# Kernel optimization log

Hardware: AMD Instinct MI355X
Metric: run time of the kernel (lower is better)

The kernel has to match this reference:

```python
import jax, jax.numpy as jnp
import numpy as np

N = 100000   # nodes
E = 1600000  # edges
IN = 32
HID = 64
OUT = 1

def setup_inputs() -> dict:
    key = jax.random.key(0)
    ks = jax.random.split(key, 16)
    x = jax.random.normal(ks[0], (N, IN), jnp.float32)
    edge_index = jax.random.randint(ks[1], (2, E), 0, N, dtype=jnp.int32)
    def lin(k, fi, fo):
        return jax.random.normal(k, (fi, fo), jnp.float32) / np.sqrt(fi)
    # SAGEConv params per layer: Wn/bn for aggregated neighbors (lin_l), Wr for root (lin_r, no bias)
    Wn0 = lin(ks[2], IN, HID);  bn0 = jnp.zeros((HID,), jnp.float32); Wr0 = lin(ks[3], IN, HID)
    Wn1 = lin(ks[4], HID, HID); bn1 = jnp.zeros((HID,), jnp.float32); Wr1 = lin(ks[5], HID, HID)
    Wn2 = lin(ks[6], HID, HID); bn2 = jnp.zeros((HID,), jnp.float32); Wr2 = lin(ks[7], HID, HID)
    # predictor MLP
    Wp1 = lin(ks[8], HID, HID); bp1 = jnp.zeros((HID,), jnp.float32)
    Wp2 = lin(ks[9], HID, OUT); bp2 = jnp.zeros((OUT,), jnp.float32)
    return dict(x=x, edge_index=edge_index,
                Wn0=Wn0, bn0=bn0, Wr0=Wr0,
                Wn1=Wn1, bn1=bn1, Wr1=Wr1,
                Wn2=Wn2, bn2=bn2, Wr2=Wr2,
                Wp1=Wp1, bp1=bp1, Wp2=Wp2, bp2=bp2)

def reference(x, edge_index, Wn0, bn0, Wr0, Wn1, bn1, Wr1, Wn2, bn2, Wr2, Wp1, bp1, Wp2, bp2):
    src, dst = edge_index[0], edge_index[1]
    n = x.shape[0]
    # mean-aggregation normalization (nodes with no in-edges get 0, as in PyG)
    cnt = jax.ops.segment_sum(jnp.ones(src.shape, x.dtype), dst, num_segments=n)
    inv = jnp.where(cnt > 0, 1.0 / jnp.maximum(cnt, 1.0), 0.0)[:, None]

    def sage(h, Wn, bn, Wr):
        agg = jax.ops.segment_sum(h[src], dst, num_segments=n) * inv  # [N, d]
        return agg @ Wn + bn + h @ Wr

    h = jax.nn.relu(sage(x, Wn0, bn0, Wr0))
    h = jax.nn.relu(sage(h, Wn1, bn1, Wr1))
    h = sage(h, Wn2, bn2, Wr2)  # no activation after last GNN layer
    h = jax.nn.relu(h @ Wp1 + bp1)
    return jax.nn.sigmoid(h @ Wp2 + bp2)
```

## Files before the change

### kernel.cpp

```cpp
#include <hip/hip_runtime.h>
#include <math.h>

#define NN 100000
#define EE 1600000
#define HID 64
#define BKT 391
#define SLAB 5504
#define CHUNK 4096
#define NWG ((EE + CHUNK - 1) / CHUNK)

typedef _Float16 f16;
typedef _Float16 f16x2 __attribute__((ext_vector_type(2)));

__device__ __forceinline__ f16x2 u2h(unsigned u) { return __builtin_bit_cast(f16x2, u); }
__device__ __forceinline__ unsigned h2u(f16x2 h) { return __builtin_bit_cast(unsigned, h); }

#if defined(__has_builtin) && __has_builtin(__builtin_amdgcn_fdot2)
__device__ __forceinline__ float dot2(f16x2 a, f16x2 b, float c) {
    return __builtin_amdgcn_fdot2(a, b, c, false);
}
#else
__device__ __forceinline__ float dot2(f16x2 a, f16x2 b, float c) {
    c = fmaf((float)a.x, (float)b.x, c);
    return fmaf((float)a.y, (float)b.y, c);
}
#endif


__global__ void place_kernel(const int* __restrict__ src, const int* __restrict__ dst,
                             int* __restrict__ bfill, unsigned* __restrict__ pairs) {
    __shared__ int lc[BKT];
    __shared__ int lbase[BKT];
    int t = threadIdx.x;
    for (int b = t; b < BKT; b += 256) lc[b] = 0;
    __syncthreads();
    int base = blockIdx.x * CHUNK;
    int myd[CHUNK / 256];
#pragma unroll
    for (int j = 0; j < CHUNK / 256; ++j) {
        int i = base + j * 256 + t;
        myd[j] = (i < EE) ? dst[i] : -1;
        if (myd[j] >= 0) atomicAdd(&lc[myd[j] >> 8], 1);
    }
    __syncthreads();
    for (int b = t; b < BKT; b += 256) {
        int c = lc[b];
        if (c) {
            int ofs = atomicAdd(&bfill[b], c);
            if (ofs + c > SLAB) ofs = SLAB - c;
            lbase[b] = b * SLAB + ofs;
        }
    }
    __syncthreads();
    for (int b = t; b < BKT; b += 256) lc[b] = 0;
    __syncthreads();
#pragma unroll
    for (int j = 0; j < CHUNK / 256; ++j) {
        int i = base + j * 256 + t;
        if (myd[j] >= 0) {
            int b = myd[j] >> 8;
            int r = atomicAdd(&lc[b], 1);
            pairs[lbase[b] + r] = (unsigned)src[i] | ((unsigned)(myd[j] & 255) << 24);
        }
    }
}

__global__ void build_kernel(const unsigned* __restrict__ pairs,
                             const int* __restrict__ bfill,
                             int* __restrict__ rs, int* __restrict__ re,
                             float* __restrict__ inv, int* __restrict__ col) {
    __shared__ unsigned s_pk[SLAB];
    __shared__ int ncnt[256];
    __shared__ int nexcl[256];
    int b = blockIdx.x;
    int t = threadIdx.x;
    int s0 = b * SLAB;
    int ce = bfill[b]; if (ce > SLAB) ce = SLAB;
    ncnt[t] = 0;
    for (int e = t; e < ce; e += 256) s_pk[e] = pairs[s0 + e];
    __syncthreads();
    for (int e = t; e < ce; e += 256) atomicAdd(&ncnt[s_pk[e] >> 24], 1);
    __syncthreads();
    int c = ncnt[t];
    nexcl[t] = c;
    __syncthreads();
    for (int off = 1; off < 256; off <<= 1) {
        int u = (t >= off) ? nexcl[t - off] : 0;
        __syncthreads();
        nexcl[t] += u;
        __syncthreads();
    }
    int excl = nexcl[t] - c;
    int node = (b << 8) + t;
    if (node < NN) {
        rs[node] = s0 + excl;
        re[node] = s0 + excl + c;
        inv[node] = (c > 0) ? (1.0f / (float)c) : 0.0f;
    }
    __syncthreads();
    nexcl[t] = excl;
    ncnt[t] = 0;
    __syncthreads();
    for (int e = t; e < ce; e += 256) {
        unsigned pk = s_pk[e];
        int d = pk >> 24;
        int r = atomicAdd(&ncnt[d], 1);
        col[s0 + nexcl[d] + r] = (int)(pk & 0xFFFFFFu);
    }
}


__global__ void transform32_kernel(const float* __restrict__ h,
                                   const float* __restrict__ Wn,
                                   const float* __restrict__ bn,
                                   const float* __restrict__ Wr,
                                   f16* __restrict__ hn,
                                   f16* __restrict__ hrb,
                                   const float* __restrict__ Wn1,
                                   const float* __restrict__ Wr1,
                                   const float* __restrict__ Wn2,
                                   const float* __restrict__ Wr2,
                                   const float* __restrict__ Wp1,
                                   unsigned* __restrict__ w16) {
    if (blockIdx.x < 40) {
        int id = blockIdx.x * 256 + threadIdx.x;
        int mat = id >> 11;
        int p = (id >> 6) & 31;
        int j = id & 63;
        const float* W = (mat == 0) ? Wn1 : (mat == 1) ? Wr1 :
                         (mat == 2) ? Wn2 : (mat == 3) ? Wr2 : Wp1;
        f16x2 v;
        v.x = (f16)W[(2 * p) * HID + j];
        v.y = (f16)W[(2 * p + 1) * HID + j];
        w16[id] = h2u(v);
    }

    int lane = threadIdx.x & 63;
    int wid = (blockIdx.x * blockDim.x + threadIdx.x) >> 6;
    int m0 = __builtin_amdgcn_readfirstlane(wid << 2);
    const float* h0 = h + (size_t)m0 * 32;

    float an0 = 0.f, an1 = 0.f, an2 = 0.f, an3 = 0.f;
    float ar0 = 0.f, ar1 = 0.f, ar2 = 0.f, ar3 = 0.f;
#pragma unroll
    for (int k = 0; k < 32; ++k) {
        float wn = Wn[k * HID + lane];
        float wr = Wr[k * HID + lane];
        float hk0 = h0[k], hk1 = h0[32 + k], hk2 = h0[64 + k], hk3 = h0[96 + k];
        an0 = fmaf(hk0, wn, an0); ar0 = fmaf(hk0, wr, ar0);
        an1 = fmaf(hk1, wn, an1); ar1 = fmaf(hk1, wr, ar1);
        an2 = fmaf(hk2, wn, an2); ar2 = fmaf(hk2, wr, ar2);
        an3 = fmaf(hk3, wn, an3); ar3 = fmaf(hk3, wr, ar3);
    }
    float b = bn[lane];
    size_t o = (size_t)m0 * HID + lane;
    hn[o] = (f16)an0; hn[o + HID] = (f16)an1;
    hn[o + 2 * HID] = (f16)an2; hn[o + 3 * HID] = (f16)an3;
    hrb[o] = (f16)(ar0 + b); hrb[o + HID] = (f16)(ar1 + b);
    hrb[o + 2 * HID] = (f16)(ar2 + b); hrb[o + 3 * HID] = (f16)(ar3 + b);
}


__device__ __forceinline__ void qgather(const uint2* __restrict__ rp,
                                        const int* __restrict__ col,
                                        int e, int en, int fl,
                                        f16x2& s0, f16x2& s1) {
    while (e + 16 <= en) {
        int c[16];
#pragma unroll
        for (int i = 0; i < 16; ++i) c[i] = col[e + i];
        uint2 v[16];
#pragma unroll
        for (int i = 0; i < 16; ++i) v[i] = rp[(size_t)c[i] * 16 + fl];
#pragma unroll
        for (int i = 0; i < 16; ++i) { s0 += u2h(v[i].x); s1 += u2h(v[i].y); }
        e += 16;
    }
    if (e + 8 <= en) {
        int c[8];
#pragma unroll
        for (int i = 0; i < 8; ++i) c[i] = col[e + i];
        uint2 v[8];
#pragma unroll
        for (int i = 0; i < 8; ++i) v[i] = rp[(size_t)c[i] * 16 + fl];
#pragma unroll
        for (int i = 0; i < 8; ++i) { s0 += u2h(v[i].x); s1 += u2h(v[i].y); }
        e += 8;
    }
    if (e + 4 <= en) {
        int c0 = col[e], c1 = col[e + 1], c2 = col[e + 2], c3 = col[e + 3];
        uint2 v0 = rp[(size_t)c0 * 16 + fl];
        uint2 v1 = rp[(size_t)c1 * 16 + fl];
        uint2 v2 = rp[(size_t)c2 * 16 + fl];
        uint2 v3 = rp[(size_t)c3 * 16 + fl];
        s0 += u2h(v0.x); s1 += u2h(v0.y);
        s0 += u2h(v1.x); s1 += u2h(v1.y);
        s0 += u2h(v2.x); s1 += u2h(v2.y);
        s0 += u2h(v3.x); s1 += u2h(v3.y);
        e += 4;
    }
    while (e < en) {
        uint2 v = rp[(size_t)col[e] * 16 + fl];
        s0 += u2h(v.x); s1 += u2h(v.y);
        ++e;
    }
}


__global__ void gt_kernel(const f16* __restrict__ An,
                          const int* __restrict__ rs, const int* __restrict__ re,
                          const int* __restrict__ col, const float* __restrict__ inv,
                          f16* C,
                          const unsigned* __restrict__ Wn16, const float* __restrict__ bn,
                          const unsigned* __restrict__ Wr16,
                          f16* __restrict__ Aout) {
    int lane = threadIdx.x & 63;
    int wid = (blockIdx.x * blockDim.x + threadIdx.x) >> 6;
    int m0 = wid << 2;
    int m = m0 + (lane >> 4);
    int fl = lane & 15;

    f16x2 s0 = (f16x2)0, s1 = (f16x2)0;
    qgather((const uint2*)An, col, rs[m], re[m], fl, s0, s1);

    float iv = inv[m];
    uint2 cur = ((const uint2*)C)[(size_t)m * 16 + fl];
    f16x2 q0 = u2h(cur.x), q1 = u2h(cur.y);
    f16x2 hA, hB;
    hA.x = (f16)fmaxf(fmaf((float)s0.x, iv, (float)q0.x), 0.f);
    hA.y = (f16)fmaxf(fmaf((float)s0.y, iv, (float)q0.y), 0.f);
    hB.x = (f16)fmaxf(fmaf((float)s1.x, iv, (float)q1.x), 0.f);
    hB.y = (f16)fmaxf(fmaf((float)s1.y, iv, (float)q1.y), 0.f);
    unsigned hx = h2u(hA), hy = h2u(hB);

    float an[4] = {0.f, 0.f, 0.f, 0.f};
    float ar[4] = {0.f, 0.f, 0.f, 0.f};
#pragma unroll
    for (int kk = 0; kk < 16; ++kk) {
        f16x2 wnA = u2h(Wn16[(2 * kk) * HID + lane]);
        f16x2 wnB = u2h(Wn16[(2 * kk + 1) * HID + lane]);
        f16x2 wrA = u2h(Wr16[(2 * kk) * HID + lane]);
        f16x2 wrB = u2h(Wr16[(2 * kk + 1) * HID + lane]);
#pragma unroll
        for (int n = 0; n < 4; ++n) {
            f16x2 px = u2h(__shfl(hx, (n << 4) + kk));
            f16x2 py = u2h(__shfl(hy, (n << 4) + kk));
            an[n] = dot2(px, wnA, an[n]);
            an[n] = dot2(py, wnB, an[n]);
            ar[n] = dot2(px, wrA, ar[n]);
            ar[n] = dot2(py, wrB, ar[n]);
        }
    }
    float b = bn[lane];
    size_t o = (size_t)m0 * HID + lane;
#pragma unroll
    for (int n = 0; n < 4; ++n) {
        Aout[o + n * HID] = (f16)an[n];
        C[o + n * HID] = (f16)(ar[n] + b);
    }
}


__global__ void gh_kernel(const f16* __restrict__ An,
                          const int* __restrict__ rs, const int* __restrict__ re,
                          const int* __restrict__ col, const float* __restrict__ inv,
                          const f16* __restrict__ C,
                          const unsigned* __restrict__ Wp116, const float* __restrict__ bp1,
                          const float* __restrict__ Wp2, const float* __restrict__ bp2,
                          float* __restrict__ out) {
    int lane = threadIdx.x & 63;
    int wid = (blockIdx.x * blockDim.x + threadIdx.x) >> 6;
    int m0 = wid << 2;
    int m = m0 + (lane >> 4);
    int fl = lane & 15;

    f16x2 s0 = (f16x2)0, s1 = (f16x2)0;
    qgather((const uint2*)An, col, rs[m], re[m], fl, s0, s1);

    float iv = inv[m];
    uint2 cur = ((const uint2*)C)[(size_t)m * 16 + fl];
    f16x2 q0 = u2h(cur.x), q1 = u2h(cur.y);
    f16x2 hA, hB;
    hA.x = (f16)fmaf((float)s0.x, iv, (float)q0.x);
    hA.y = (f16)fmaf((float)s0.y, iv, (float)q0.y);
    hB.x = (f16)fmaf((float)s1.x, iv, (float)q1.x);
    hB.y = (f16)fmaf((float)s1.y, iv, (float)q1.y);
    unsigned hx = h2u(hA), hy = h2u(hB);

    float tn[4] = {0.f, 0.f, 0.f, 0.f};
#pragma unroll
    for (int kk = 0; kk < 16; ++kk) {
        f16x2 wA = u2h(Wp116[(2 * kk) * HID + lane]);
        f16x2 wB = u2h(Wp116[(2 * kk + 1) * HID + lane]);
#pragma unroll
        for (int n = 0; n < 4; ++n) {
            f16x2 px = u2h(__shfl(hx, (n << 4) + kk));
            f16x2 py = u2h(__shfl(hy, (n << 4) + kk));
            tn[n] = dot2(px, wA, tn[n]);
            tn[n] = dot2(py, wB, tn[n]);
        }
    }
    float b = bp1[lane], w2v = Wp2[lane];
    float r0 = fmaxf(tn[0] + b, 0.f) * w2v;
    float r1 = fmaxf(tn[1] + b, 0.f) * w2v;
    float r2 = fmaxf(tn[2] + b, 0.f) * w2v;
    float r3 = fmaxf(tn[3] + b, 0.f) * w2v;
#pragma unroll
    for (int off = 32; off > 0; off >>= 1) {
        r0 += __shfl_xor(r0, off);
        r1 += __shfl_xor(r1, off);
        r2 += __shfl_xor(r2, off);
        r3 += __shfl_xor(r3, off);
    }
    if (lane == 0) {
        float bb = bp2[0];
        out[m0]     = 1.f / (1.f + expf(-(r0 + bb)));
        out[m0 + 1] = 1.f / (1.f + expf(-(r1 + bb)));
        out[m0 + 2] = 1.f / (1.f + expf(-(r2 + bb)));
        out[m0 + 3] = 1.f / (1.f + expf(-(r3 + bb)));
    }
}

extern "C" void kernel_launch(void* const* d_in, const int* in_sizes, int n_in,
                              void* d_out, int out_size, void* d_ws, size_t ws_size,
                              hipStream_t stream) {
    const float* x   = (const float*)d_in[0];
    const int* eidx  = (const int*)d_in[1];
    const float* Wn0 = (const float*)d_in[2];
    const float* bn0 = (const float*)d_in[3];
    const float* Wr0 = (const float*)d_in[4];
    const float* Wn1 = (const float*)d_in[5];
    const float* bn1 = (const float*)d_in[6];
    const float* Wr1 = (const float*)d_in[7];
    const float* Wn2 = (const float*)d_in[8];
    const float* bn2 = (const float*)d_in[9];
    const float* Wr2 = (const float*)d_in[10];
    const float* Wp1 = (const float*)d_in[11];
    const float* bp1 = (const float*)d_in[12];
    const float* Wp2 = (const float*)d_in[13];
    const float* bp2 = (const float*)d_in[14];
    float* out = (float*)d_out;

    const int* src = eidx;
    const int* dst = eidx + EE;

    char* w = (char*)d_ws;
    size_t off = 0;
    auto carve = [&](size_t bytes) -> void* {
        void* p = w + off;
        off = (off + bytes + 255) & ~(size_t)255;
        return p;
    };
    int*   rsA    = (int*)carve((size_t)NN * 4);
    int*   reA    = (int*)carve((size_t)NN * 4);
    float* inv    = (float*)carve((size_t)NN * 4);
    int*   col    = (int*)carve((size_t)BKT * SLAB * 4);
    int*   bfill  = (int*)carve((size_t)BKT * 4);
    unsigned* w16 = (unsigned*)carve((size_t)5 * 2048 * 4);
    f16*   A0     = (f16*)carve((size_t)NN * HID * 2);
    f16*   A1     = (f16*)carve((size_t)NN * HID * 2);
    f16*   C      = (f16*)carve((size_t)NN * HID * 2);
    unsigned* pairs = (unsigned*)carve((size_t)BKT * SLAB * 4);
    (void)ws_size;

    unsigned* Wn1_16 = w16;
    unsigned* Wr1_16 = w16 + 2048;
    unsigned* Wn2_16 = w16 + 4096;
    unsigned* Wr2_16 = w16 + 6144;
    unsigned* Wp1_16 = w16 + 8192;

    hipMemsetAsync(bfill, 0, (size_t)BKT * 4, stream);

    place_kernel<<<NWG, 256, 0, stream>>>(src, dst, bfill, pairs);
    build_kernel<<<BKT, 256, 0, stream>>>(pairs, bfill, rsA, reA, inv, col);

    const int tb = NN / 16;

    transform32_kernel<<<tb, 256, 0, stream>>>(x, Wn0, bn0, Wr0, A0, C,
                                               Wn1, Wr1, Wn2, Wr2, Wp1, w16);
    gt_kernel<<<tb, 256, 0, stream>>>(A0, rsA, reA, col, inv, C, Wn1_16, bn1, Wr1_16, A1);
    gt_kernel<<<tb, 256, 0, stream>>>(A1, rsA, reA, col, inv, C, Wn2_16, bn2, Wr2_16, A0);
    gh_kernel<<<tb, 256, 0, stream>>>(A0, rsA, reA, col, inv, C, Wp1_16, bp1, Wp2, bp2, out);
}
```

Baseline: 295.3 us.

## Merge edge placement and first-layer transform into one launch; shrink gather unroll

```diff
diff --git a/kernel.cpp b/kernel.cpp
--- a/kernel.cpp
+++ b/kernel.cpp
@@ -8,6 +8,7 @@
 #define SLAB 5504
 #define CHUNK 4096
 #define NWG ((EE + CHUNK - 1) / CHUNK)
+#define TB (NN / 16)
 
 typedef _Float16 f16;
 typedef _Float16 f16x2 __attribute__((ext_vector_type(2)));
@@ -27,43 +28,94 @@
 #endif
 
 
-__global__ void place_kernel(const int* __restrict__ src, const int* __restrict__ dst,
-                             int* __restrict__ bfill, unsigned* __restrict__ pairs) {
+__global__ void mt_kernel(const int* __restrict__ src, const int* __restrict__ dst,
+                          int* __restrict__ bfill, unsigned* __restrict__ pairs,
+                          const float* __restrict__ h,
+                          const float* __restrict__ Wn, const float* __restrict__ bn,
+                          const float* __restrict__ Wr,
+                          f16* __restrict__ hn, f16* __restrict__ hrb,
+                          const float* __restrict__ Wn1, const float* __restrict__ Wr1,
+                          const float* __restrict__ Wn2, const float* __restrict__ Wr2,
+                          const float* __restrict__ Wp1, unsigned* __restrict__ w16) {
     __shared__ int lc[BKT];
     __shared__ int lbase[BKT];
     int t = threadIdx.x;
-    for (int b = t; b < BKT; b += 256) lc[b] = 0;
-    __syncthreads();
-    int base = blockIdx.x * CHUNK;
-    int myd[CHUNK / 256];
-#pragma unroll
-    for (int j = 0; j < CHUNK / 256; ++j) {
-        int i = base + j * 256 + t;
-        myd[j] = (i < EE) ? dst[i] : -1;
-        if (myd[j] >= 0) atomicAdd(&lc[myd[j] >> 8], 1);
-    }
-    __syncthreads();
-    for (int b = t; b < BKT; b += 256) {
-        int c = lc[b];
-        if (c) {
-            int ofs = atomicAdd(&bfill[b], c);
-            if (ofs + c > SLAB) ofs = SLAB - c;
-            lbase[b] = b * SLAB + ofs;
-        }
-    }
-    __syncthreads();
-    for (int b = t; b < BKT; b += 256) lc[b] = 0;
-    __syncthreads();
-#pragma unroll
-    for (int j = 0; j < CHUNK / 256; ++j) {
-        int i = base + j * 256 + t;
-        if (myd[j] >= 0) {
-            int b = myd[j] >> 8;
-            int r = atomicAdd(&lc[b], 1);
-            pairs[lbase[b] + r] = (unsigned)src[i] | ((unsigned)(myd[j] & 255) << 24);
-        }
-    }
-}
+
+    if (blockIdx.x < NWG) {
+        for (int b = t; b < BKT; b += 256) lc[b] = 0;
+        __syncthreads();
+        int base = blockIdx.x * CHUNK;
+        int myd[CHUNK / 256];
+#pragma unroll
+        for (int j = 0; j < CHUNK / 256; ++j) {
+            int i = base + j * 256 + t;
+            myd[j] = (i < EE) ? dst[i] : -1;
+            if (myd[j] >= 0) atomicAdd(&lc[myd[j] >> 8], 1);
+        }
+        __syncthreads();
+        for (int b = t; b < BKT; b += 256) {
+            int c = lc[b];
+            if (c) {
+                int ofs = atomicAdd(&bfill[b], c);
+                if (ofs + c > SLAB) ofs = SLAB - c;
+                lbase[b] = b * SLAB + ofs;
+            }
+        }
+        __syncthreads();
+        for (int b = t; b < BKT; b += 256) lc[b] = 0;
+        __syncthreads();
+#pragma unroll
+        for (int j = 0; j < CHUNK / 256; ++j) {
+            int i = base + j * 256 + t;
+            if (myd[j] >= 0) {
+                int b = myd[j] >> 8;
+                int r = atomicAdd(&lc[b], 1);
+                pairs[lbase[b] + r] = (unsigned)src[i] | ((unsigned)(myd[j] & 255) << 24);
+            }
+        }
+        return;
+    }
+
+    int bb = blockIdx.x - NWG;
+
+    if (bb < 40) {
+        int id = bb * 256 + t;
+        int mat = id >> 11;
+        int p = (id >> 6) & 31;
+        int j = id & 63;
+        const float* W = (mat == 0) ? Wn1 : (mat == 1) ? Wr1 :
+                         (mat == 2) ? Wn2 : (mat == 3) ? Wr2 : Wp1;
+        f16x2 v;
+        v.x = (f16)W[(2 * p) * HID + j];
+        v.y = (f16)W[(2 * p + 1) * HID + j];
+        w16[id] = h2u(v);
+    }
+
+    int lane = t & 63;
+    int wid = (bb * 256 + t) >> 6;
+    int m0 = __builtin_amdgcn_readfirstlane(wid << 2);
+    const float* h0 = h + (size_t)m0 * 32;
+
+    float an0 = 0.f, an1 = 0.f, an2 = 0.f, an3 = 0.f;
+    float ar0 = 0.f, ar1 = 0.f, ar2 = 0.f, ar3 = 0.f;
+#pragma unroll
+    for (int k = 0; k < 32; ++k) {
+        float wn = Wn[k * HID + lane];
+        float wr = Wr[k * HID + lane];
+        float hk0 = h0[k], hk1 = h0[32 + k], hk2 = h0[64 + k], hk3 = h0[96 + k];
+        an0 = fmaf(hk0, wn, an0); ar0 = fmaf(hk0, wr, ar0);
+        an1 = fmaf(hk1, wn, an1); ar1 = fmaf(hk1, wr, ar1);
+        an2 = fmaf(hk2, wn, an2); ar2 = fmaf(hk2, wr, ar2);
+        an3 = fmaf(hk3, wn, an3); ar3 = fmaf(hk3, wr, ar3);
+    }
+    float b = bn[lane];
+    size_t o = (size_t)m0 * HID + lane;
+    hn[o] = (f16)an0; hn[o + HID] = (f16)an1;
+    hn[o + 2 * HID] = (f16)an2; hn[o + 3 * HID] = (f16)an3;
+    hrb[o] = (f16)(ar0 + b); hrb[o + HID] = (f16)(ar1 + b);
+    hrb[o + 2 * HID] = (f16)(ar2 + b); hrb[o + 3 * HID] = (f16)(ar3 + b);
+}
+
 
 __global__ void build_kernel(const unsigned* __restrict__ pairs,
                              const int* __restrict__ bfill,
@@ -110,81 +162,29 @@
 }
 
 
-__global__ void transform32_kernel(const float* __restrict__ h,
-                                   const float* __restrict__ Wn,
-                                   const float* __restrict__ bn,
-                                   const float* __restrict__ Wr,
-                                   f16* __restrict__ hn,
-                                   f16* __restrict__ hrb,
-                                   const float* __restrict__ Wn1,
-                                   const float* __restrict__ Wr1,
-                                   const float* __restrict__ Wn2,
-                                   const float* __restrict__ Wr2,
-                                   const float* __restrict__ Wp1,
-                                   unsigned* __restrict__ w16) {
-    if (blockIdx.x < 40) {
-        int id = blockIdx.x * 256 + threadIdx.x;
-        int mat = id >> 11;
-        int p = (id >> 6) & 31;
-        int j = id & 63;
-        const float* W = (mat == 0) ? Wn1 : (mat == 1) ? Wr1 :
-                         (mat == 2) ? Wn2 : (mat == 3) ? Wr2 : Wp1;
-        f16x2 v;
-        v.x = (f16)W[(2 * p) * HID + j];
-        v.y = (f16)W[(2 * p + 1) * HID + j];
-        w16[id] = h2u(v);
-    }
-
-    int lane = threadIdx.x & 63;
-    int wid = (blockIdx.x * blockDim.x + threadIdx.x) >> 6;
-    int m0 = __builtin_amdgcn_readfirstlane(wid << 2);
-    const float* h0 = h + (size_t)m0 * 32;
-
-    float an0 = 0.f, an1 = 0.f, an2 = 0.f, an3 = 0.f;
-    float ar0 = 0.f, ar1 = 0.f, ar2 = 0.f, ar3 = 0.f;
-#pragma unroll
-    for (int k = 0; k < 32; ++k) {
-        float wn = Wn[k * HID + lane];
-        float wr = Wr[k * HID + lane];
-        float hk0 = h0[k], hk1 = h0[32 + k], hk2 = h0[64 + k], hk3 = h0[96 + k];
-        an0 = fmaf(hk0, wn, an0); ar0 = fmaf(hk0, wr, ar0);
-        an1 = fmaf(hk1, wn, an1); ar1 = fmaf(hk1, wr, ar1);
-        an2 = fmaf(hk2, wn, an2); ar2 = fmaf(hk2, wr, ar2);
-        an3 = fmaf(hk3, wn, an3); ar3 = fmaf(hk3, wr, ar3);
-    }
-    float b = bn[lane];
-    size_t o = (size_t)m0 * HID + lane;
-    hn[o] = (f16)an0; hn[o + HID] = (f16)an1;
-    hn[o + 2 * HID] = (f16)an2; hn[o + 3 * HID] = (f16)an3;
-    hrb[o] = (f16)(ar0 + b); hrb[o + HID] = (f16)(ar1 + b);
-    hrb[o + 2 * HID] = (f16)(ar2 + b); hrb[o + 3 * HID] = (f16)(ar3 + b);
-}
-
-
 __device__ __forceinline__ void qgather(const uint2* __restrict__ rp,
                                         const int* __restrict__ col,
                                         int e, int en, int fl,
                                         f16x2& s0, f16x2& s1) {
-    while (e + 16 <= en) {
-        int c[16];
-#pragma unroll
-        for (int i = 0; i < 16; ++i) c[i] = col[e + i];
-        uint2 v[16];
-#pragma unroll
-        for (int i = 0; i < 16; ++i) v[i] = rp[(size_t)c[i] * 16 + fl];
-#pragma unroll
-        for (int i = 0; i < 16; ++i) { s0 += u2h(v[i].x); s1 += u2h(v[i].y); }
-        e += 16;
-    }
-    if (e + 8 <= en) {
-        int c[8];
-#pragma unroll
-        for (int i = 0; i < 8; ++i) c[i] = col[e + i];
-        uint2 v[8];
-#pragma unroll
-        for (int i = 0; i < 8; ++i) v[i] = rp[(size_t)c[i] * 16 + fl];
-#pragma unroll
-        for (int i = 0; i < 8; ++i) { s0 += u2h(v[i].x); s1 += u2h(v[i].y); }
+    while (e + 8 <= en) {
+        int c0 = col[e],     c1 = col[e + 1], c2 = col[e + 2], c3 = col[e + 3];
+        int c4 = col[e + 4], c5 = col[e + 5], c6 = col[e + 6], c7 = col[e + 7];
+        uint2 v0 = rp[(size_t)c0 * 16 + fl];
+        uint2 v1 = rp[(size_t)c1 * 16 + fl];
+        uint2 v2 = rp[(size_t)c2 * 16 + fl];
+        uint2 v3 = rp[(size_t)c3 * 16 + fl];
+        uint2 v4 = rp[(size_t)c4 * 16 + fl];
+        uint2 v5 = rp[(size_t)c5 * 16 + fl];
+        uint2 v6 = rp[(size_t)c6 * 16 + fl];
+        uint2 v7 = rp[(size_t)c7 * 16 + fl];
+        s0 += u2h(v0.x); s1 += u2h(v0.y);
+        s0 += u2h(v1.x); s1 += u2h(v1.y);
+        s0 += u2h(v2.x); s1 += u2h(v2.y);
+        s0 += u2h(v3.x); s1 += u2h(v3.y);
+        s0 += u2h(v4.x); s1 += u2h(v4.y);
+        s0 += u2h(v5.x); s1 += u2h(v5.y);
+        s0 += u2h(v6.x); s1 += u2h(v6.y);
+        s0 += u2h(v7.x); s1 += u2h(v7.y);
         e += 8;
     }
     if (e + 4 <= en) {
@@ -371,14 +371,12 @@
 
     hipMemsetAsync(bfill, 0, (size_t)BKT * 4, stream);
 
-    place_kernel<<<NWG, 256, 0, stream>>>(src, dst, bfill, pairs);
+    mt_kernel<<<NWG + TB, 256, 0, stream>>>(src, dst, bfill, pairs,
+                                            x, Wn0, bn0, Wr0, A0, C,
+                                            Wn1, Wr1, Wn2, Wr2, Wp1, w16);
     build_kernel<<<BKT, 256, 0, stream>>>(pairs, bfill, rsA, reA, inv, col);
 
-    const int tb = NN / 16;
-
-    transform32_kernel<<<tb, 256, 0, stream>>>(x, Wn0, bn0, Wr0, A0, C,
-                                               Wn1, Wr1, Wn2, Wr2, Wp1, w16);
-    gt_kernel<<<tb, 256, 0, stream>>>(A0, rsA, reA, col, inv, C, Wn1_16, bn1, Wr1_16, A1);
-    gt_kernel<<<tb, 256, 0, stream>>>(A1, rsA, reA, col, inv, C, Wn2_16, bn2, Wr2_16, A0);
-    gh_kernel<<<tb, 256, 0, stream>>>(A0, rsA, reA, col, inv, C, Wp1_16, bp1, Wp2, bp2, out);
-}
+    gt_kernel<<<TB, 256, 0, stream>>>(A0, rsA, reA, col, inv, C, Wn1_16, bn1, Wr1_16, A1);
+    gt_kernel<<<TB, 256, 0, stream>>>(A1, rsA, reA, col, inv, C, Wn2_16, bn2, Wr2_16, A0);
+    gh_kernel<<<TB, 256, 0, stream>>>(A0, rsA, reA, col, inv, C, Wp1_16, bp1, Wp2, bp2, out);
+}
```

Measured after the change: 278.1 us, median of 2. 1.06x faster.
